# Kernel tuning notes

Measured on AMD Instinct MI355X. Metric: run time of the kernel, lower is better.

## Reference

```python
import jax, jax.numpy as jnp
import numpy as np

NUM_HEADS = 16


def setup_inputs() -> dict:
    key = jax.random.key(0)
    ks = jax.random.split(key, 9)
    B, N, C, R, T = 16, 1024, 1024, 64, 10
    s = 0.02
    x = jax.random.normal(ks[0], (B, N, C), dtype=jnp.float32)
    W_qkv = jax.random.normal(ks[1], (3 * C, C), dtype=jnp.float32) * s
    W_proj = jax.random.normal(ks[2], (C, C), dtype=jnp.float32) * s
    b_proj = jax.random.normal(ks[3], (C,), dtype=jnp.float32) * s
    A_k = jax.random.normal(ks[4], (T, R, C), dtype=jnp.float32) * s
    B_k = jax.random.normal(ks[5], (T, C, R), dtype=jnp.float32) * s
    A_v = jax.random.normal(ks[6], (T, R, C), dtype=jnp.float32) * s
    B_v = jax.random.normal(ks[7], (T, C, R), dtype=jnp.float32) * s
    return {"x": x, "W_qkv": W_qkv, "W_proj": W_proj, "b_proj": b_proj,
            "A_k": A_k, "B_k": B_k, "A_v": A_v, "B_v": B_v, "task": 4}


def reference(x, W_qkv, W_proj, b_proj, A_k, B_k, A_v, B_v, task):
    B, N, C = x.shape
    H = NUM_HEADS
    hd = C // H
    scale = hd ** (-0.5)

    # qkv projection: x @ W_qkv.T -> [B,N,3C] -> [3,B,H,N,hd]
    qkv = (x @ W_qkv.T).reshape(B, N, 3, H, hd).transpose(2, 0, 3, 1, 4)
    q, k, v = qkv[0], qkv[1], qkv[2]

    # merged LoRA weights: sum_{t<=task} B[t] @ A[t] -> [C, C]
    w_k = jnp.einsum('tcr,trd->cd', B_k[:task + 1], A_k[:task + 1])
    w_v = jnp.einsum('tcr,trd->cd', B_v[:task + 1], A_v[:task + 1])
    # F.linear(x, W) = x @ W.T ; reshape to [B,H,N,hd]
    dk = (x @ w_k.T).reshape(B, N, H, hd).transpose(0, 2, 1, 3)
    dv = (x @ w_v.T).reshape(B, N, H, hd).transpose(0, 2, 1, 3)
    k = k + dk
    v = v + dv

    attn = jax.nn.softmax(jnp.einsum('bhnd,bhmd->bhnm', q, k) * scale, axis=-1)
    out = jnp.einsum('bhnm,bhmd->bhnd', attn, v)
    out = out.transpose(0, 2, 1, 3).reshape(B, N, C)
    return out @ W_proj.T + b_proj
```

## Files before the change

### kernel.cpp

```cpp
#include <hip/hip_runtime.h>

typedef __attribute__((ext_vector_type(4))) float f32x4;
typedef __attribute__((ext_vector_type(8))) short s16x8;
typedef __attribute__((ext_vector_type(2))) unsigned int u32x2;
typedef __attribute__((ext_vector_type(4))) unsigned int u32x4;

#define LOG2E 1.44269504088896340736f

__device__ inline unsigned short f2b(float f) {
  unsigned int u = __float_as_uint(f);
  unsigned int r = (u + 0x7FFFu + ((u >> 16) & 1u)) >> 16;
  return (unsigned short)r;
}

__device__ inline unsigned int cvtpk_bf16(float lo, float hi) {
  unsigned int r;
  asm("v_cvt_pk_bf16_f32 %0, %1, %2" : "=v"(r) : "v"(lo), "v"(hi));
  return r;
}

__device__ inline void gload_lds16(const unsigned short* g, unsigned short* l) {
  __builtin_amdgcn_global_load_lds(
      (const __attribute__((address_space(1))) unsigned int*)g,
      (__attribute__((address_space(3))) unsigned int*)l, 16, 0, 0);
}

__global__ __launch_bounds__(256) void lora_merge(const float* __restrict__ A_k,
                                                  const float* __restrict__ B_k,
                                                  const float* __restrict__ A_v,
                                                  const float* __restrict__ B_v,
                                                  float* __restrict__ wk,
                                                  float* __restrict__ wv,
                                                  const int* __restrict__ taskp) {
  const float* A_ = blockIdx.y ? A_v : A_k;
  const float* B_ = blockIdx.y ? B_v : B_k;
  float* Wd = blockIdx.y ? wv : wk;
  __shared__ float Bs[64][65];
  __shared__ float As[64][65];
  const int tile = blockIdx.x;
  const int c0 = (tile >> 4) * 64, d0 = (tile & 15) * 64;
  const int tid = threadIdx.x;
  const int tx = tid & 15, ty = tid >> 4;
  const int T = *taskp + 1;
  float acc[4][4] = {};
  const int r = tid >> 2, cb = (tid & 3) * 16;
  for (int t = 0; t < T; ++t) {
    __syncthreads();
    const float* srcB = B_ + (size_t)t * 65536 + (size_t)(c0 + r) * 64 + cb;
    const float* srcA = A_ + (size_t)t * 65536 + (size_t)r * 1024 + d0 + cb;
#pragma unroll
    for (int j = 0; j < 16; j += 4) {
      f32x4 vb = *(const f32x4*)(srcB + j);
      Bs[r][cb + j] = vb.x; Bs[r][cb + j + 1] = vb.y;
      Bs[r][cb + j + 2] = vb.z; Bs[r][cb + j + 3] = vb.w;
      f32x4 va = *(const f32x4*)(srcA + j);
      As[r][cb + j] = va.x; As[r][cb + j + 1] = va.y;
      As[r][cb + j + 2] = va.z; As[r][cb + j + 3] = va.w;
    }
    __syncthreads();
#pragma unroll 8
    for (int rr = 0; rr < 64; ++rr) {
      float bv[4], av[4];
#pragma unroll
      for (int i = 0; i < 4; ++i) bv[i] = Bs[ty * 4 + i][rr];
#pragma unroll
      for (int j = 0; j < 4; ++j) av[j] = As[rr][tx * 4 + j];
#pragma unroll
      for (int i = 0; i < 4; ++i)
#pragma unroll
        for (int j = 0; j < 4; ++j) acc[i][j] += bv[i] * av[j];
    }
  }
#pragma unroll
  for (int i = 0; i < 4; ++i)
#pragma unroll
    for (int j = 0; j < 4; ++j)
      Wd[(size_t)(c0 + ty * 4 + i) * 1024 + d0 + tx * 4 + j] = acc[i][j];
}

__global__ void prep_cvt(const float* __restrict__ x, const float* __restrict__ Wproj,
                         unsigned short* __restrict__ xb, unsigned short* __restrict__ Wp) {
  int i = blockIdx.x * 256 + threadIdx.x;
  const float* src;
  unsigned short* dst;
  int idx;
  if (i < 4194304) { src = x; dst = xb; idx = i; }
  else { idx = i - 4194304; if (idx >= 262144) return; src = Wproj; dst = Wp; }
  f32x4 v = ((const f32x4*)src)[idx];
  unsigned short o0 = f2b(v.x), o1 = f2b(v.y), o2 = f2b(v.z), o3 = f2b(v.w);
  unsigned long long pack = (unsigned long long)o0 | ((unsigned long long)o1 << 16) |
                            ((unsigned long long)o2 << 32) | ((unsigned long long)o3 << 48);
  ((unsigned long long*)dst)[idx] = pack;
}

__global__ void build_wc(const float* __restrict__ Wqkv, const float* __restrict__ wk,
                         const float* __restrict__ wv, unsigned short* __restrict__ Wc) {
  int i = blockIdx.x * 256 + threadIdx.x;
  int e = i * 4;
  f32x4 v = *(const f32x4*)(Wqkv + e);
  int row = e >> 10;
  if (row >= 2048) {
    f32x4 d = *(const f32x4*)(wv + (e - 2097152));
    v = v + d;
  } else if (row >= 1024) {
    f32x4 d = *(const f32x4*)(wk + (e - 1048576));
    v = v + d;
  }
  unsigned short o0 = f2b(v.x), o1 = f2b(v.y), o2 = f2b(v.z), o3 = f2b(v.w);
  unsigned long long pack = (unsigned long long)o0 | ((unsigned long long)o1 << 16) |
                            ((unsigned long long)o2 << 32) | ((unsigned long long)o3 << 48);
  ((unsigned long long*)Wc)[i] = pack;
}

template <int OUT_BF16, int ADD_BIAS>
__global__ __launch_bounds__(512, 1) void gemm256(const unsigned short* __restrict__ A,
                                                  const unsigned short* __restrict__ B,
                                                  void* __restrict__ Cout,
                                                  const float* __restrict__ bias,
                                                  int M, int N, int K) {
  __shared__ unsigned short SA[4][8192];
  __shared__ unsigned short SB[4][8192];
  const int tid = threadIdx.x;
  const int w = tid >> 6, l = tid & 63;
  const int lr = l & 15, lg = l >> 4;
  const int wm = w >> 2, wn = w & 3;

  const int lin = blockIdx.y * gridDim.x + blockIdx.x;
  const int cpx = (gridDim.x * gridDim.y) >> 3;
  const int s = (lin & 7) * cpx + (lin >> 3);
  const int bx = s % gridDim.x, by = s / gridDim.x;

  const int cs = tid ^ (((tid >> 5) & 1) << 1);
  const int r_st = ((cs >> 6) << 4) | ((cs >> 2) & 15);
  const int k_st = (cs & 3) << 3;
  const unsigned short* gA0 = A + (size_t)(by * 256 + r_st) * K + k_st;
  const unsigned short* gA1 = A + (size_t)(by * 256 + 128 + r_st) * K + k_st;
  const unsigned short* gB0 = B + (size_t)(bx * 256 + r_st) * K + k_st;
  const unsigned short* gB1 = B + (size_t)(bx * 256 + 128 + r_st) * K + k_st;
  const int wb = w * 512;

  const int swz = ((lr >> 3) & 1) << 4;
  const int fbase = lr * 32 + lg * 8;
  const int hA = wm * 4096;
  const int hB = (wn >> 1) * 4096;
  const int nb = (wn & 1) * 4;

  f32x4 acc[8][4] = {};
  const int NT = K >> 5;

#pragma unroll
  for (int t = 0; t < 3; ++t) {
    gload_lds16(gA0 + t * 32, &SA[t][wb]);
    gload_lds16(gA1 + t * 32, &SA[t][4096 + wb]);
    gload_lds16(gB0 + t * 32, &SB[t][wb]);
    gload_lds16(gB1 + t * 32, &SB[t][4096 + wb]);
  }
  asm volatile("s_waitcnt vmcnt(8)" ::: "memory");
  __builtin_amdgcn_s_barrier();
  __builtin_amdgcn_sched_barrier(0);

  for (int t = 0; t < NT; ++t) {
    const int slot = t & 3;
    const int ts = (t + 3 < NT) ? (t + 3) : (NT - 1);
    const int ssl = (t + 3) & 3;
    const unsigned short* sa = &SA[slot][hA];
    const unsigned short* sb = &SB[slot][hB];
    s16x8 af[8], bf[2];
#pragma unroll
    for (int m = 0; m < 8; ++m)
      af[m] = *(const s16x8*)&sa[(m * 512 + fbase) ^ swz];
#pragma unroll
    for (int n = 0; n < 2; ++n)
      bf[n] = *(const s16x8*)&sb[((nb + n) * 512 + fbase) ^ swz];
    gload_lds16(gA0 + ts * 32, &SA[ssl][wb]);
    gload_lds16(gA1 + ts * 32, &SA[ssl][4096 + wb]);
    __builtin_amdgcn_s_barrier();
    asm volatile("s_waitcnt lgkmcnt(0)" ::: "memory");
    __builtin_amdgcn_sched_barrier(0);
    __builtin_amdgcn_s_setprio(1);
#pragma unroll
    for (int m = 0; m < 8; ++m)
#pragma unroll
      for (int n = 0; n < 2; ++n)
        acc[m][n] = __builtin_amdgcn_mfma_f32_16x16x32_bf16(af[m], bf[n], acc[m][n], 0, 0, 0);
    __builtin_amdgcn_s_setprio(0);
    __builtin_amdgcn_sched_barrier(0);
    __builtin_amdgcn_s_barrier();
#pragma unroll
    for (int n = 0; n < 2; ++n)
      bf[n] = *(const s16x8*)&sb[((nb + 2 + n) * 512 + fbase) ^ swz];
    gload_lds16(gB0 + ts * 32, &SB[ssl][wb]);
    gload_lds16(gB1 + ts * 32, &SB[ssl][4096 + wb]);
    __builtin_amdgcn_s_barrier();
    asm volatile("s_waitcnt lgkmcnt(0)" ::: "memory");
    __builtin_amdgcn_sched_barrier(0);
    __builtin_amdgcn_s_setprio(1);
#pragma unroll
    for (int m = 0; m < 8; ++m)
#pragma unroll
      for (int n = 0; n < 2; ++n)
        acc[m][2 + n] = __builtin_amdgcn_mfma_f32_16x16x32_bf16(af[m], bf[n], acc[m][2 + n], 0, 0, 0);
    __builtin_amdgcn_s_setprio(0);
    __builtin_amdgcn_sched_barrier(0);
    asm volatile("s_waitcnt vmcnt(8)" ::: "memory");
    __builtin_amdgcn_s_barrier();
    __builtin_amdgcn_sched_barrier(0);
  }

  const int crow0 = by * 256 + wm * 128;
  const int ccol0 = bx * 256 + wn * 64;
  if (OUT_BF16) {
    unsigned short* C = (unsigned short*)Cout;
#pragma unroll
    for (int m = 0; m < 8; ++m)
#pragma unroll
      for (int n = 0; n < 4; ++n)
#pragma unroll
        for (int rr = 0; rr < 4; ++rr) {
          int row = crow0 + m * 16 + lg * 4 + rr;
          int col = ccol0 + n * 16 + lr;
          C[(size_t)row * N + col] = f2b(acc[m][n][rr]);
        }
  } else {
    float* C = (float*)Cout;
#pragma unroll
    for (int m = 0; m < 8; ++m)
#pragma unroll
      for (int n = 0; n < 4; ++n)
#pragma unroll
        for (int rr = 0; rr < 4; ++rr) {
          int row = crow0 + m * 16 + lg * 4 + rr;
          int col = ccol0 + n * 16 + lr;
          float b = ADD_BIAS ? bias[col] : 0.f;
          C[(size_t)row * N + col] = acc[m][n][rr] + b;
        }
  }
}

__global__ __launch_bounds__(64) void transpose_v(const unsigned short* __restrict__ qkv,
                                                  unsigned short* __restrict__ vT) {
  __shared__ unsigned short T[64 * 65];
  const int bh = blockIdx.x >> 4;
  const int nt = blockIdx.x & 15;
  const int b = bh >> 4, h = bh & 15;
  const int l = threadIdx.x;
  const unsigned short* src = qkv + (size_t)(b * 1024 + nt * 64) * 3072 + 2048 + h * 64;
#pragma unroll
  for (int p = 0; p < 8; ++p) {
    int slot = p * 64 + l;
    int n = slot >> 3, dc = (slot & 7) * 8;
    u32x4 v = *(const u32x4*)(src + (size_t)n * 3072 + dc);
    const unsigned short* vs = (const unsigned short*)&v;
#pragma unroll
    for (int j = 0; j < 8; ++j) T[n * 65 + dc + j] = vs[j];
  }
  __syncthreads();
  unsigned short* dst = vT + (size_t)bh * 65536 + nt * 64;
#pragma unroll
  for (int p = 0; p < 8; ++p) {
    int slot = p * 64 + l;
    int d = slot >> 3, nc = (slot & 7) * 8;
    union { unsigned short s[8]; u32x4 v; } tmp;
#pragma unroll
    for (int j = 0; j < 8; ++j) tmp.s[j] = T[(nc + j) * 65 + d];
    *(u32x4*)(dst + (size_t)d * 1024 + nc) = tmp.v;
  }
}

__global__ __launch_bounds__(512) void attn_fwd(const unsigned short* __restrict__ qkv,
                                                const unsigned short* __restrict__ vT,
                                                unsigned short* __restrict__ out) {
  const int tid = threadIdx.x;
  const int w = tid >> 6, l = tid & 63;
  const int lr = l & 15, lg = l >> 4;
  const int bid = blockIdx.x;
  const int g = (bid & 7) * 32 + (bid >> 5);
  const int qt2 = (bid >> 3) & 3;
  const int b = g >> 4, h = g & 15;

  __shared__ unsigned short Ks[2][4096];
  __shared__ unsigned short Vs[2][4096];
  __shared__ unsigned int Ps[16][576];

  const size_t base = (size_t)b * 1024 * 3072 + h * 64;
  const unsigned short* Qp = qkv + base;
  const unsigned short* Kp = qkv + base + 1024;
  const unsigned short* vTp = vT + (size_t)(b * 16 + h) * 65536;

  const float SSCALE = 0.125f * LOG2E;
  const int qb = qt2 * 256;
  s16x8 qf[2][2];
#pragma unroll
  for (int qg = 0; qg < 2; ++qg) {
    const int qrow = qb + qg * 128 + w * 16 + lr;
    qf[qg][0] = *(const s16x8*)(Qp + (size_t)qrow * 3072 + lg * 8);
    qf[qg][1] = *(const s16x8*)(Qp + (size_t)qrow * 3072 + 32 + lg * 8);
#pragma unroll
    for (int kk = 0; kk < 2; ++kk)
#pragma unroll
      for (int j = 0; j < 8; ++j) {
        float f = __uint_as_float(((unsigned int)(unsigned short)qf[qg][kk][j]) << 16) * SSCALE;
        qf[qg][kk][j] = (short)f2b(f);
      }
  }

  s16x8 ONES;
#pragma unroll
  for (int j = 0; j < 8; ++j) ONES[j] = (short)0x3F80;

  f32x4 o[2][4] = {};
  f32x4 o4[2] = {};

  const int srow = tid >> 3;
  const int csrc = (tid & 7) ^ (srow & 7);

  gload_lds16(Kp + (size_t)srow * 3072 + csrc * 8, &Ks[0][w * 512]);
  gload_lds16(vTp + (size_t)srow * 1024 + csrc * 8, &Vs[0][w * 512]);
  __syncthreads();

  for (int t = 0; t < 16; ++t) {
    const int cur = t & 1;
    if (t < 15) {
      const int kv1 = (t + 1) * 64;
      gload_lds16(Kp + (size_t)(kv1 + srow) * 3072 + csrc * 8, &Ks[cur ^ 1][w * 512]);
      gload_lds16(vTp + (size_t)srow * 1024 + kv1 + csrc * 8, &Vs[cur ^ 1][w * 512]);
    }
    const unsigned short* Kb = &Ks[cur][0];
    const unsigned short* Vb = &Vs[cur][0];

    f32x4 sc[2][4] = {};
    __builtin_amdgcn_s_setprio(1);
#pragma unroll
    for (int kk = 0; kk < 2; ++kk)
#pragma unroll
      for (int tt = 0; tt < 4; ++tt) {
        int krow = tt * 16 + lr;
        s16x8 kf = *(const s16x8*)&Kb[krow * 64 + ((((kk * 32 + lg * 8) >> 3) ^ (krow & 7)) << 3)];
        sc[0][tt] = __builtin_amdgcn_mfma_f32_16x16x32_bf16(kf, qf[0][kk], sc[0][tt], 0, 0, 0);
        sc[1][tt] = __builtin_amdgcn_mfma_f32_16x16x32_bf16(kf, qf[1][kk], sc[1][tt], 0, 0, 0);
      }
    __builtin_amdgcn_s_setprio(0);

#pragma unroll
    for (int qg = 0; qg < 2; ++qg) {
      unsigned int* Pw = &Ps[(w << 1) | qg][0];
#pragma unroll
      for (int tt = 0; tt < 4; ++tt) {
        float p0 = exp2f(sc[qg][tt][0]);
        float p1 = exp2f(sc[qg][tt][1]);
        float p2 = exp2f(sc[qg][tt][2]);
        float p3 = exp2f(sc[qg][tt][3]);
        u32x2 pk;
        pk.x = cvtpk_bf16(p0, p1);
        pk.y = cvtpk_bf16(p2, p3);
        *(u32x2*)&Pw[lr * 36 + tt * 8 + lg * 2] = pk;
      }
    }
    __builtin_amdgcn_sched_barrier(0);

#pragma unroll
    for (int kk = 0; kk < 2; ++kk) {
      u32x4 pu0 = *(const u32x4*)&Ps[(w << 1)][lr * 36 + kk * 16 + lg * 4];
      u32x4 pu1 = *(const u32x4*)&Ps[(w << 1) | 1][lr * 36 + kk * 16 + lg * 4];
      s16x8 pf0 = __builtin_bit_cast(s16x8, pu0);
      s16x8 pf1 = __builtin_bit_cast(s16x8, pu1);
      __builtin_amdgcn_s_setprio(1);
      o4[0] = __builtin_amdgcn_mfma_f32_16x16x32_bf16(pf0, ONES, o4[0], 0, 0, 0);
      o4[1] = __builtin_amdgcn_mfma_f32_16x16x32_bf16(pf1, ONES, o4[1], 0, 0, 0);
#pragma unroll
      for (int dt = 0; dt < 4; ++dt) {
        int vrow = dt * 16 + lr;
        s16x8 vf = *(const s16x8*)&Vb[vrow * 64 + ((((kk * 32 + lg * 8) >> 3) ^ (vrow & 7)) << 3)];
        o[0][dt] = __builtin_amdgcn_mfma_f32_16x16x32_bf16(pf0, vf, o[0][dt], 0, 0, 0);
        o[1][dt] = __builtin_amdgcn_mfma_f32_16x16x32_bf16(pf1, vf, o[1][dt], 0, 0, 0);
      }
      __builtin_amdgcn_s_setprio(0);
    }
    __syncthreads();
  }

#pragma unroll
  for (int qg = 0; qg < 2; ++qg) {
    f32x4 lq;
#pragma unroll
    for (int rr = 0; rr < 4; ++rr) lq[rr] = 1.f / o4[qg][rr];
    const size_t orow0 = (size_t)b * 1024 + qb + qg * 128 + w * 16;
#pragma unroll
    for (int dt = 0; dt < 4; ++dt)
#pragma unroll
      for (int rr = 0; rr < 4; ++rr)
        out[(orow0 + lg * 4 + rr) * 1024 + h * 64 + dt * 16 + lr] = f2b(o[qg][dt][rr] * lq[rr]);
  }
}

extern "C" void kernel_launch(void* const* d_in, const int* in_sizes, int n_in,
                              void* d_out, int out_size, void* d_ws, size_t ws_size,
                              hipStream_t stream) {
  const float* x = (const float*)d_in[0];
  const float* Wqkv = (const float*)d_in[1];
  const float* Wproj = (const float*)d_in[2];
  const float* bproj = (const float*)d_in[3];
  const float* A_k = (const float*)d_in[4];
  const float* B_k = (const float*)d_in[5];
  const float* A_v = (const float*)d_in[6];
  const float* B_v = (const float*)d_in[7];
  const int* task = (const int*)d_in[8];

  char* ws = (char*)d_ws;
  float* wk = (float*)ws;
  float* wv = (float*)(ws + (4ull << 20));
  unsigned short* xb = (unsigned short*)(ws + (8ull << 20));
  unsigned short* Wc = (unsigned short*)(ws + (40ull << 20));
  unsigned short* Wp = (unsigned short*)(ws + (46ull << 20));
  unsigned short* qkv = (unsigned short*)(ws + (48ull << 20));
  unsigned short* ao = (unsigned short*)(ws + (144ull << 20));
  unsigned short* vT = xb;

  lora_merge<<<dim3(256, 2), 256, 0, stream>>>(A_k, B_k, A_v, B_v, wk, wv, task);
  prep_cvt<<<17408, 256, 0, stream>>>(x, Wproj, xb, Wp);
  build_wc<<<3072, 256, 0, stream>>>(Wqkv, wk, wv, Wc);
  gemm256<1, 0><<<dim3(12, 64), 512, 0, stream>>>(xb, Wc, qkv, nullptr, 16384, 3072, 1024);
  transpose_v<<<4096, 64, 0, stream>>>(qkv, vT);
  attn_fwd<<<1024, 512, 0, stream>>>(qkv, vT, ao);
  gemm256<0, 1><<<dim3(4, 64), 512, 0, stream>>>(ao, Wp, d_out, bproj, 16384, 1024, 1024);
}
```

Measured before the change: 331.1 us.

## Fuse V transpose into QKV GEMM epilogue and merge prep kernels

The QKV GEMM epilogue now writes Q and K into separate contiguous buffers and, for V column tiles, transposes through shared memory and writes V^T directly. This removes the standalone transpose_v kernel and its extra read and write of V. The weight conversion and combined-weight build kernels are merged into one launch, saving a launch. Attention now reads Q and K with a 1024 stride instead of 3072. V tiles pay an extra LDS staging step and barriers in the epilogue.

```diff
diff --git a/kernel.cpp b/kernel.cpp
--- a/kernel.cpp
+++ b/kernel.cpp
@@ -78,48 +78,48 @@
       Wd[(size_t)(c0 + ty * 4 + i) * 1024 + d0 + tx * 4 + j] = acc[i][j];
 }
 
-__global__ void prep_cvt(const float* __restrict__ x, const float* __restrict__ Wproj,
-                         unsigned short* __restrict__ xb, unsigned short* __restrict__ Wp) {
+__global__ void prep_all(const float* __restrict__ x, const float* __restrict__ Wproj,
+                         const float* __restrict__ Wqkv, const float* __restrict__ wk,
+                         const float* __restrict__ wv, unsigned short* __restrict__ xb,
+                         unsigned short* __restrict__ Wp, unsigned short* __restrict__ Wc) {
   int i = blockIdx.x * 256 + threadIdx.x;
-  const float* src;
+  f32x4 v;
   unsigned short* dst;
   int idx;
-  if (i < 4194304) { src = x; dst = xb; idx = i; }
-  else { idx = i - 4194304; if (idx >= 262144) return; src = Wproj; dst = Wp; }
-  f32x4 v = ((const f32x4*)src)[idx];
+  if (i < 4194304) {
+    idx = i; dst = xb;
+    v = ((const f32x4*)x)[idx];
+  } else if (i < 4456448) {
+    idx = i - 4194304; dst = Wp;
+    v = ((const f32x4*)Wproj)[idx];
+  } else {
+    idx = i - 4456448;
+    dst = Wc;
+    int e = idx * 4;
+    v = *(const f32x4*)(Wqkv + e);
+    int row = e >> 10;
+    if (row >= 2048) {
+      f32x4 d = *(const f32x4*)(wv + (e - 2097152));
+      v = v + d;
+    } else if (row >= 1024) {
+      f32x4 d = *(const f32x4*)(wk + (e - 1048576));
+      v = v + d;
+    }
+  }
   unsigned short o0 = f2b(v.x), o1 = f2b(v.y), o2 = f2b(v.z), o3 = f2b(v.w);
   unsigned long long pack = (unsigned long long)o0 | ((unsigned long long)o1 << 16) |
                             ((unsigned long long)o2 << 32) | ((unsigned long long)o3 << 48);
   ((unsigned long long*)dst)[idx] = pack;
 }
 
-__global__ void build_wc(const float* __restrict__ Wqkv, const float* __restrict__ wk,
-                         const float* __restrict__ wv, unsigned short* __restrict__ Wc) {
-  int i = blockIdx.x * 256 + threadIdx.x;
-  int e = i * 4;
-  f32x4 v = *(const f32x4*)(Wqkv + e);
-  int row = e >> 10;
-  if (row >= 2048) {
-    f32x4 d = *(const f32x4*)(wv + (e - 2097152));
-    v = v + d;
-  } else if (row >= 1024) {
-    f32x4 d = *(const f32x4*)(wk + (e - 1048576));
-    v = v + d;
-  }
-  unsigned short o0 = f2b(v.x), o1 = f2b(v.y), o2 = f2b(v.z), o3 = f2b(v.w);
-  unsigned long long pack = (unsigned long long)o0 | ((unsigned long long)o1 << 16) |
-                            ((unsigned long long)o2 << 32) | ((unsigned long long)o3 << 48);
-  ((unsigned long long*)Wc)[i] = pack;
-}
-
-template <int OUT_BF16, int ADD_BIAS>
+template <int OUT_BF16, int ADD_BIAS, int VFUSE>
 __global__ __launch_bounds__(512, 1) void gemm256(const unsigned short* __restrict__ A,
                                                   const unsigned short* __restrict__ B,
                                                   void* __restrict__ Cout,
                                                   const float* __restrict__ bias,
+                                                  unsigned short* __restrict__ Vt,
                                                   int M, int N, int K) {
-  __shared__ unsigned short SA[4][8192];
-  __shared__ unsigned short SB[4][8192];
+  __shared__ unsigned short SM[65536];
   const int tid = threadIdx.x;
   const int w = tid >> 6, l = tid & 63;
   const int lr = l & 15, lg = l >> 4;
@@ -148,12 +148,15 @@
   f32x4 acc[8][4] = {};
   const int NT = K >> 5;
 
+#define SA_(t) (&SM[(t) * 8192])
+#define SB_(t) (&SM[32768 + (t) * 8192])
+
 #pragma unroll
   for (int t = 0; t < 3; ++t) {
-    gload_lds16(gA0 + t * 32, &SA[t][wb]);
-    gload_lds16(gA1 + t * 32, &SA[t][4096 + wb]);
-    gload_lds16(gB0 + t * 32, &SB[t][wb]);
-    gload_lds16(gB1 + t * 32, &SB[t][4096 + wb]);
+    gload_lds16(gA0 + t * 32, SA_(t) + wb);
+    gload_lds16(gA1 + t * 32, SA_(t) + 4096 + wb);
+    gload_lds16(gB0 + t * 32, SB_(t) + wb);
+    gload_lds16(gB1 + t * 32, SB_(t) + 4096 + wb);
   }
   asm volatile("s_waitcnt vmcnt(8)" ::: "memory");
   __builtin_amdgcn_s_barrier();
@@ -163,8 +166,8 @@
     const int slot = t & 3;
     const int ts = (t + 3 < NT) ? (t + 3) : (NT - 1);
     const int ssl = (t + 3) & 3;
-    const unsigned short* sa = &SA[slot][hA];
-    const unsigned short* sb = &SB[slot][hB];
+    const unsigned short* sa = SA_(slot) + hA;
+    const unsigned short* sb = SB_(slot) + hB;
     s16x8 af[8], bf[2];
 #pragma unroll
     for (int m = 0; m < 8; ++m)
@@ -172,8 +175,8 @@
 #pragma unroll
     for (int n = 0; n < 2; ++n)
       bf[n] = *(const s16x8*)&sb[((nb + n) * 512 + fbase) ^ swz];
-    gload_lds16(gA0 + ts * 32, &SA[ssl][wb]);
-    gload_lds16(gA1 + ts * 32, &SA[ssl][4096 + wb]);
+    gload_lds16(gA0 + ts * 32, SA_(ssl) + wb);
+    gload_lds16(gA1 + ts * 32, SA_(ssl) + 4096 + wb);
     __builtin_amdgcn_s_barrier();
     asm volatile("s_waitcnt lgkmcnt(0)" ::: "memory");
     __builtin_amdgcn_sched_barrier(0);
@@ -189,8 +192,8 @@
 #pragma unroll
     for (int n = 0; n < 2; ++n)
       bf[n] = *(const s16x8*)&sb[((nb + 2 + n) * 512 + fbase) ^ swz];
-    gload_lds16(gB0 + ts * 32, &SB[ssl][wb]);
-    gload_lds16(gB1 + ts * 32, &SB[ssl][4096 + wb]);
+    gload_lds16(gB0 + ts * 32, SB_(ssl) + wb);
+    gload_lds16(gB1 + ts * 32, SB_(ssl) + 4096 + wb);
     __builtin_amdgcn_s_barrier();
     asm volatile("s_waitcnt lgkmcnt(0)" ::: "memory");
     __builtin_amdgcn_sched_barrier(0);
@@ -209,7 +212,58 @@
 
   const int crow0 = by * 256 + wm * 128;
   const int ccol0 = bx * 256 + wn * 64;
-  if (OUT_BF16) {
+
+  if (VFUSE) {
+    unsigned short* Cq = (unsigned short*)Cout;
+    if (bx < 8) {
+      unsigned short* Cb = Cq + ((size_t)((ccol0 >> 10) & 1)) * 16777216;
+#pragma unroll
+      for (int m = 0; m < 8; ++m)
+#pragma unroll
+        for (int n = 0; n < 4; ++n)
+#pragma unroll
+          for (int rr = 0; rr < 4; ++rr) {
+            int row = crow0 + m * 16 + lg * 4 + rr;
+            int col = (ccol0 + n * 16 + lr) & 1023;
+            Cb[(size_t)row * 1024 + col] = f2b(acc[m][n][rr]);
+          }
+    } else {
+      asm volatile("s_waitcnt vmcnt(0)" ::: "memory");
+      __syncthreads();
+      unsigned int* T32 = (unsigned int*)SM;
+      const int h0 = (bx - 8) * 4;
+      const int bb = by >> 2;
+      const int n_base = (by & 3) * 256;
+#pragma unroll
+      for (int hf = 0; hf < 2; ++hf) {
+        if (wm == hf) {
+#pragma unroll
+          for (int m = 0; m < 8; ++m)
+#pragma unroll
+            for (int n = 0; n < 4; ++n) {
+              int lcol = wn * 64 + n * 16 + lr;
+              u32x2 pk;
+              pk.x = (unsigned int)f2b(acc[m][n][0]) | ((unsigned int)f2b(acc[m][n][1]) << 16);
+              pk.y = (unsigned int)f2b(acc[m][n][2]) | ((unsigned int)f2b(acc[m][n][3]) << 16);
+              *(u32x2*)&T32[lcol * 68 + m * 8 + lg * 2] = pk;
+            }
+        }
+        __syncthreads();
+#pragma unroll
+        for (int p = 0; p < 8; ++p) {
+          int slot2 = p * 512 + tid;
+          int d256 = slot2 >> 4;
+          int ncq = (slot2 & 15) * 4;
+          u32x4 v = *(const u32x4*)&T32[d256 * 68 + ncq];
+          int hloc = d256 >> 6, d = d256 & 63;
+          size_t dst = (size_t)(bb * 16 + h0 + hloc) * 65536 + (size_t)d * 1024 +
+                       (n_base + hf * 128 + ncq * 2);
+          *(u32x4*)&Vt[dst] = v;
+        }
+        __syncthreads();
+      }
+    }
+  } else if (OUT_BF16) {
     unsigned short* C = (unsigned short*)Cout;
 #pragma unroll
     for (int m = 0; m < 8; ++m)
@@ -235,39 +289,12 @@
           C[(size_t)row * N + col] = acc[m][n][rr] + b;
         }
   }
-}
-
-__global__ __launch_bounds__(64) void transpose_v(const unsigned short* __restrict__ qkv,
-                                                  unsigned short* __restrict__ vT) {
-  __shared__ unsigned short T[64 * 65];
-  const int bh = blockIdx.x >> 4;
-  const int nt = blockIdx.x & 15;
-  const int b = bh >> 4, h = bh & 15;
-  const int l = threadIdx.x;
-  const unsigned short* src = qkv + (size_t)(b * 1024 + nt * 64) * 3072 + 2048 + h * 64;
-#pragma unroll
-  for (int p = 0; p < 8; ++p) {
-    int slot = p * 64 + l;
-    int n = slot >> 3, dc = (slot & 7) * 8;
-    u32x4 v = *(const u32x4*)(src + (size_t)n * 3072 + dc);
-    const unsigned short* vs = (const unsigned short*)&v;
-#pragma unroll
-    for (int j = 0; j < 8; ++j) T[n * 65 + dc + j] = vs[j];
-  }
-  __syncthreads();
-  unsigned short* dst = vT + (size_t)bh * 65536 + nt * 64;
-#pragma unroll
-  for (int p = 0; p < 8; ++p) {
-    int slot = p * 64 + l;
-    int d = slot >> 3, nc = (slot & 7) * 8;
-    union { unsigned short s[8]; u32x4 v; } tmp;
-#pragma unroll
-    for (int j = 0; j < 8; ++j) tmp.s[j] = T[(nc + j) * 65 + d];
-    *(u32x4*)(dst + (size_t)d * 1024 + nc) = tmp.v;
-  }
-}
-
-__global__ __launch_bounds__(512) void attn_fwd(const unsigned short* __restrict__ qkv,
+#undef SA_
+#undef SB_
+}
+
+__global__ __launch_bounds__(512) void attn_fwd(const unsigned short* __restrict__ Qb,
+                                                const unsigned short* __restrict__ Kb,
                                                 const unsigned short* __restrict__ vT,
                                                 unsigned short* __restrict__ out) {
   const int tid = threadIdx.x;
@@ -282,9 +309,9 @@
   __shared__ unsigned short Vs[2][4096];
   __shared__ unsigned int Ps[16][576];
 
-  const size_t base = (size_t)b * 1024 * 3072 + h * 64;
-  const unsigned short* Qp = qkv + base;
-  const unsigned short* Kp = qkv + base + 1024;
+  const size_t base = (size_t)b * 1048576 + h * 64;
+  const unsigned short* Qp = Qb + base;
+  const unsigned short* Kp = Kb + base;
   const unsigned short* vTp = vT + (size_t)(b * 16 + h) * 65536;
 
   const float SSCALE = 0.125f * LOG2E;
@@ -293,8 +320,8 @@
 #pragma unroll
   for (int qg = 0; qg < 2; ++qg) {
     const int qrow = qb + qg * 128 + w * 16 + lr;
-    qf[qg][0] = *(const s16x8*)(Qp + (size_t)qrow * 3072 + lg * 8);
-    qf[qg][1] = *(const s16x8*)(Qp + (size_t)qrow * 3072 + 32 + lg * 8);
+    qf[qg][0] = *(const s16x8*)(Qp + (size_t)qrow * 1024 + lg * 8);
+    qf[qg][1] = *(const s16x8*)(Qp + (size_t)qrow * 1024 + 32 + lg * 8);
 #pragma unroll
     for (int kk = 0; kk < 2; ++kk)
 #pragma unroll
@@ -314,7 +341,7 @@
   const int srow = tid >> 3;
   const int csrc = (tid & 7) ^ (srow & 7);
 
-  gload_lds16(Kp + (size_t)srow * 3072 + csrc * 8, &Ks[0][w * 512]);
+  gload_lds16(Kp + (size_t)srow * 1024 + csrc * 8, &Ks[0][w * 512]);
   gload_lds16(vTp + (size_t)srow * 1024 + csrc * 8, &Vs[0][w * 512]);
   __syncthreads();
 
@@ -322,10 +349,10 @@
     const int cur = t & 1;
     if (t < 15) {
       const int kv1 = (t + 1) * 64;
-      gload_lds16(Kp + (size_t)(kv1 + srow) * 3072 + csrc * 8, &Ks[cur ^ 1][w * 512]);
+      gload_lds16(Kp + (size_t)(kv1 + srow) * 1024 + csrc * 8, &Ks[cur ^ 1][w * 512]);
       gload_lds16(vTp + (size_t)srow * 1024 + kv1 + csrc * 8, &Vs[cur ^ 1][w * 512]);
     }
-    const unsigned short* Kb = &Ks[cur][0];
+    const unsigned short* Kb_ = &Ks[cur][0];
     const unsigned short* Vb = &Vs[cur][0];
 
     f32x4 sc[2][4] = {};
@@ -335,7 +362,7 @@
 #pragma unroll
       for (int tt = 0; tt < 4; ++tt) {
         int krow = tt * 16 + lr;
-        s16x8 kf = *(const s16x8*)&Kb[krow * 64 + ((((kk * 32 + lg * 8) >> 3) ^ (krow & 7)) << 3)];
+        s16x8 kf = *(const s16x8*)&Kb_[krow * 64 + ((((kk * 32 + lg * 8) >> 3) ^ (krow & 7)) << 3)];
         sc[0][tt] = __builtin_amdgcn_mfma_f32_16x16x32_bf16(kf, qf[0][kk], sc[0][tt], 0, 0, 0);
         sc[1][tt] = __builtin_amdgcn_mfma_f32_16x16x32_bf16(kf, qf[1][kk], sc[1][tt], 0, 0, 0);
       }
@@ -412,15 +439,14 @@
   unsigned short* xb = (unsigned short*)(ws + (8ull << 20));
   unsigned short* Wc = (unsigned short*)(ws + (40ull << 20));
   unsigned short* Wp = (unsigned short*)(ws + (46ull << 20));
-  unsigned short* qkv = (unsigned short*)(ws + (48ull << 20));
+  unsigned short* Qb = (unsigned short*)(ws + (48ull << 20));
+  unsigned short* Kb = (unsigned short*)(ws + (80ull << 20));
+  unsigned short* vT = (unsigned short*)(ws + (112ull << 20));
   unsigned short* ao = (unsigned short*)(ws + (144ull << 20));
-  unsigned short* vT = xb;
 
   lora_merge<<<dim3(256, 2), 256, 0, stream>>>(A_k, B_k, A_v, B_v, wk, wv, task);
-  prep_cvt<<<17408, 256, 0, stream>>>(x, Wproj, xb, Wp);
-  build_wc<<<3072, 256, 0, stream>>>(Wqkv, wk, wv, Wc);
-  gemm256<1, 0><<<dim3(12, 64), 512, 0, stream>>>(xb, Wc, qkv, nullptr, 16384, 3072, 1024);
-  transpose_v<<<4096, 64, 0, stream>>>(qkv, vT);
-  attn_fwd<<<1024, 512, 0, stream>>>(qkv, vT, ao);
-  gemm256<0, 1><<<dim3(4, 64), 512, 0, stream>>>(ao, Wp, d_out, bproj, 16384, 1024, 1024);
-}
+  prep_all<<<20480, 256, 0, stream>>>(x, Wproj, Wqkv, wk, wv, xb, Wp, Wc);
+  gemm256<1, 0, 1><<<dim3(12, 64), 512, 0, stream>>>(xb, Wc, Qb, nullptr, vT, 16384, 3072, 1024);
+  attn_fwd<<<1024, 512, 0, stream>>>(Qb, Kb, vT, ao);
+  gemm256<0, 1, 0><<<dim3(4, 64), 512, 0, stream>>>(ao, Wp, d_out, bproj, nullptr, 16384, 1024, 1024);
+}
```

After: 311.5 us. 5.9% less time.
